# Optimization experiments

Hardware: AMD Instinct MI355X
Metric: run time of the kernel (lower is better)

## Reference

```python
import jax, jax.numpy as jnp
import numpy as np

NUM_CLASSES = 21
TOP_K = 200
CONF_THRESH = 0.01
NMS_THRESH = 0.45
VAR0, VAR1 = 0.1, 0.2
B, P = 64, 8732  # SSD300 VOC prior count


def setup_inputs() -> dict:
    key = jax.random.key(0)
    k1, k2, k3 = jax.random.split(key, 3)
    loc = jax.random.normal(k1, (B, P, 4), dtype=jnp.float32)
    conf = jax.random.normal(k2, (B, P, NUM_CLASSES), dtype=jnp.float32)
    priors = jax.random.uniform(k3, (P, 4), dtype=jnp.float32, minval=0.02, maxval=1.0)
    return {"loc": loc, "conf": conf, "priors": priors}


def _decode(loc, priors):
    # loc, priors: [P, 4] (cx, cy, w, h) offsets -> corner boxes [P, 4]
    cxcy = priors[:, :2] + loc[:, :2] * VAR0 * priors[:, 2:]
    wh = priors[:, 2:] * jnp.exp(loc[:, 2:] * VAR1)
    x1y1 = cxcy - wh * 0.5
    x2y2 = x1y1 + wh
    return jnp.concatenate([x1y1, x2y2], axis=1)


def _iou_matrix(boxes):
    # boxes [K,4] -> pairwise IoU [K,K] with the original +1 pixel convention
    x1, y1, x2, y2 = boxes[:, 0], boxes[:, 1], boxes[:, 2], boxes[:, 3]
    area = (x2 - x1 + 1.0) * (y2 - y1 + 1.0)
    xx1 = jnp.maximum(x1[:, None], x1[None, :])
    yy1 = jnp.maximum(y1[:, None], y1[None, :])
    xx2 = jnp.minimum(x2[:, None], x2[None, :])
    yy2 = jnp.minimum(y2[:, None], y2[None, :])
    w = jnp.maximum(0.0, xx2 - xx1 + 1.0)
    h = jnp.maximum(0.0, yy2 - yy1 + 1.0)
    inter = w * h
    return inter / (area[:, None] + area[None, :] - inter)


def _nms_keep(boxes, valid):
    # boxes [K,4] sorted by descending score; greedy NMS as a fixed-length loop
    K = boxes.shape[0]
    iou = _iou_matrix(boxes)
    later = jnp.arange(K)[None, :] > jnp.arange(K)[:, None]  # strictly lower-priority

    def body(i, suppressed):
        keep_i = valid[i] & ~suppressed[i]
        return suppressed | (keep_i & (iou[i] > NMS_THRESH) & later[i])

    suppressed = jax.lax.fori_loop(0, K, body, jnp.zeros((K,), bool))
    return valid & ~suppressed


def _per_class(scores, decoded):
    # scores [P], decoded [P,4] -> [TOP_K, 7] rows (score, x1, y1, x2, y2, 0, 0)
    valid_p = scores > CONF_THRESH
    s = jnp.where(valid_p, scores, -1.0)
    top_s, idx = jax.lax.top_k(s, TOP_K)
    b = decoded[idx]                      # [K,4]
    valid = top_s > CONF_THRESH
    keep = _nms_keep(b, valid)
    rows = jnp.concatenate([top_s[:, None], b], axis=1)  # [K,5]
    order = jnp.argsort(~keep)            # stable: kept rows compacted to front
    rows = jnp.where(keep[order][:, None], rows[order], 0.0)
    return jnp.pad(rows, ((0, 0), (0, 2)))  # pad to width 7 (original leaves cols 5:7 zero)


def _per_image(loc_i, conf_i, priors):
    decoded = _decode(loc_i, priors)      # [P,4]
    # classes 1..C-1 (skip background class 0)
    cls_scores = conf_i[:, 1:].T          # [C-1, P]
    cls_out = jax.vmap(lambda s: _per_class(s, decoded))(cls_scores)  # [C-1,K,7]
    bg = jnp.zeros((1, TOP_K, 7), dtype=loc_i.dtype)
    return jnp.concatenate([bg, cls_out], axis=0)  # [C,K,7]


def _detect(loc, conf, priors):
    conf_soft = jax.nn.softmax(conf, axis=-1)  # SSD test phase applies softmax
    output = jax.vmap(_per_image, in_axes=(0, 0, None))(loc, conf_soft, priors)  # [B,C,K,7]
    flt = output.reshape(output.shape[0], -1, 7)  # [B, C*K, 7]
    score = flt[:, :, 0]
    idx = jnp.argsort(-score, axis=1)
    rank = jnp.argsort(idx, axis=1)
    mask = rank < TOP_K
    order = jnp.argsort(~mask, axis=1)    # stable: top-K rows, original positional order
    sel = jnp.take_along_axis(flt, order[:, :TOP_K, None], axis=1)  # [B,K,7]
    return sel.reshape(-1, 7)             # [B*K, 7], matching flt[rank < top_k]


def reference(loc, conf, priors):
    return _detect(loc, conf, priors)
```

## Files before the change

kernel.cpp:

```cpp
#include <hip/hip_runtime.h>
#include <stdint.h>

#define NUM_P 8732
#define NUM_B 64
#define NUM_CLS 21
#define TOPK 200
#define NMS_T 0.45f
#define CONF_T 0.01f
#define NL 35
#define NV4 2183
#define NL2 16
#define MAXCAND 4000
#define ORD_SENT 0x407FFFFFu
#define HI_BITS 0x17800u

__device__ __forceinline__ uint32_t ordf(float f) {
    uint32_t u = __float_as_uint(f);
    return (u & 0x80000000u) ? ~u : (u | 0x80000000u);
}
__device__ __forceinline__ float unordf(uint32_t v) {
    uint32_t u = (v & 0x80000000u) ? (v ^ 0x80000000u) : ~v;
    return __uint_as_float(u);
}

__global__ __launch_bounds__(256) void prep_kernel(const float* __restrict__ conf,
                                                   uint32_t* __restrict__ ct,
                                                   uint32_t* __restrict__ candCount) {
    __shared__ float tile[256 * NUM_CLS];
    const int bx = blockIdx.x;
    const int b = blockIdx.y;
    const int tid = threadIdx.x;
    if (bx == 0 && b == 0 && tid < NUM_B) candCount[tid] = 0u;
    const int p0 = bx * 256;
    const int np = min(256, NUM_P - p0);
    const int nf4 = (np * NUM_CLS) / 4;
    const float4* src = reinterpret_cast<const float4*>(conf + ((size_t)b * NUM_P + p0) * NUM_CLS);
    float4* dst = reinterpret_cast<float4*>(tile);
#pragma unroll
    for (int i = 0; i < 6; ++i) {
        int idx = tid + i * 256;
        if (idx < nf4) dst[idx] = src[idx];
    }
    __syncthreads();
    if (tid < np) {
        const int p = p0 + tid;
        const float* row = tile + tid * NUM_CLS;
        float x[NUM_CLS];
#pragma unroll
        for (int c = 0; c < NUM_CLS; ++c) x[c] = row[c];
        float m = x[0];
#pragma unroll
        for (int c = 1; c < NUM_CLS; ++c) m = fmaxf(m, x[c]);
        float e[NUM_CLS];
        float s = 0.0f;
#pragma unroll
        for (int c = 0; c < NUM_CLS; ++c) { e[c] = expf(x[c] - m); s += e[c]; }
#pragma unroll
        for (int c = 1; c < NUM_CLS; ++c) {
            float sc = e[c] / s;
            float sv = (sc > CONF_T) ? sc : -1.0f;
            ct[((size_t)(b * 20 + (c - 1))) * NUM_P + p] = ordf(sv);
        }
    }
}

__global__ __launch_bounds__(256, 4) void select_nms_kernel(const uint32_t* __restrict__ ct,
                                                            const float* __restrict__ loc,
                                                            const float* __restrict__ priors,
                                                            float* __restrict__ selS,
                                                            float* __restrict__ selX1,
                                                            float* __restrict__ selY1,
                                                            float* __restrict__ selX2,
                                                            float* __restrict__ selY2,
                                                            uint64_t* __restrict__ cands,
                                                            uint32_t* __restrict__ candCount) {
    __shared__ uint32_t hist[2048];
    __shared__ uint32_t wtot[4];
    __shared__ uint32_t sh_d, sh_above, sh_bnd, sh_nsent;
    __shared__ uint64_t skey[256];
    __shared__ int scnt;
    __shared__ int sh_run;

    const int blk = blockIdx.x;
    const int b = blk / 20;
    const int c = blk % 20;
    const int tid = threadIdx.x;
    const int lane = tid & 63;
    const int wv = tid >> 6;
    const uint32_t* col = ct + (size_t)blk * NUM_P;
    const uint4* colv = reinterpret_cast<const uint4*>(col);

#pragma unroll
    for (int i = 0; i < 8; ++i) hist[tid + i * 256] = 0;
    skey[tid] = 0;
    if (tid == 0) { scnt = 0; sh_run = 0; }
    __syncthreads();

    uint4 vv[9];
#pragma unroll
    for (int i = 0; i < 9; ++i) {
        int idx = tid + i * 256;
        vv[i] = make_uint4(ORD_SENT, ORD_SENT, ORD_SENT, ORD_SENT);
        if (idx < NV4) vv[i] = colv[idx];
    }
    int nsent = 0;
#pragma unroll
    for (int i = 0; i < 9; ++i) {
        int idx = tid + i * 256;
        if (idx < NV4) {
            uint32_t a0 = vv[i].x, a1 = vv[i].y, a2 = vv[i].z, a3 = vv[i].w;
            if (a0 == ORD_SENT) nsent++; else atomicAdd(&hist[(a0 >> 15) & 2047u], 1u);
            if (a1 == ORD_SENT) nsent++; else atomicAdd(&hist[(a1 >> 15) & 2047u], 1u);
            if (a2 == ORD_SENT) nsent++; else atomicAdd(&hist[(a2 >> 15) & 2047u], 1u);
            if (a3 == ORD_SENT) nsent++; else atomicAdd(&hist[(a3 >> 15) & 2047u], 1u);
        }
    }
    {
        int v = nsent;
#pragma unroll
        for (int off = 32; off; off >>= 1) v += __shfl_down(v, off);
        if (lane == 0) wtot[wv] = (uint32_t)v;
        __syncthreads();
        if (tid == 0) sh_nsent = wtot[0] + wtot[1] + wtot[2] + wtot[3];
        __syncthreads();
    }
    const int nreal = NUM_P - (int)sh_nsent;

    uint32_t emitThr = 0;
    bool ranked = false;
    uint32_t thrEq = 0;
    int needEq = 0;

    if (nreal >= TOPK) {
        {
            const int tbase = tid * 8;
            uint32_t ls = 0;
#pragma unroll
            for (int j = 0; j < 8; ++j) ls += hist[tbase + j];
            uint32_t v = ls;
#pragma unroll
            for (int off = 1; off < 64; off <<= 1) {
                uint32_t o2 = __shfl_down(v, off);
                if (lane + off < 64) v += o2;
            }
            if (lane == 0) wtot[wv] = v;
            __syncthreads();
            uint32_t above_wave = 0;
            for (int w = wv + 1; w < 4; ++w) above_wave += wtot[w];
            uint32_t acc = (v + above_wave) - ls;
            for (int j = 7; j >= 0; --j) {
                uint32_t h = hist[tbase + j];
                if (acc < (uint32_t)TOPK && acc + h >= (uint32_t)TOPK) {
                    sh_d = (uint32_t)(tbase + j);
                    sh_above = acc;
                    sh_bnd = h;
                }
                acc += h;
            }
            __syncthreads();
        }
        uint32_t d1 = sh_d;
        int cert = (int)sh_above;
        int need = TOPK - cert;
        int bnd = (int)sh_bnd;
        const uint32_t lvl1 = HI_BITS | d1;

        if (cert + bnd <= 256) {
            emitThr = lvl1 << 15;
        } else {
            __syncthreads();
#pragma unroll
            for (int i = 0; i < 8; ++i) hist[tid + i * 256] = 0;
            __syncthreads();
#pragma unroll
            for (int i = 0; i < 9; ++i) {
                int idx = tid + i * 256;
                if (idx < NV4) {
                    if ((vv[i].x >> 15) == lvl1) atomicAdd(&hist[(vv[i].x >> 4) & 2047u], 1u);
                    if ((vv[i].y >> 15) == lvl1) atomicAdd(&hist[(vv[i].y >> 4) & 2047u], 1u);
                    if ((vv[i].z >> 15) == lvl1) atomicAdd(&hist[(vv[i].z >> 4) & 2047u], 1u);
                    if ((vv[i].w >> 15) == lvl1) atomicAdd(&hist[(vv[i].w >> 4) & 2047u], 1u);
                }
            }
            __syncthreads();
            {
                const int tbase = tid * 8;
                uint32_t ls = 0;
#pragma unroll
                for (int j = 0; j < 8; ++j) ls += hist[tbase + j];
                uint32_t v = ls;
#pragma unroll
                for (int off = 1; off < 64; off <<= 1) {
                    uint32_t o2 = __shfl_down(v, off);
                    if (lane + off < 64) v += o2;
                }
                if (lane == 0) wtot[wv] = v;
                __syncthreads();
                uint32_t above_wave = 0;
                for (int w = wv + 1; w < 4; ++w) above_wave += wtot[w];
                uint32_t acc = (v + above_wave) - ls;
                for (int j = 7; j >= 0; --j) {
                    uint32_t h = hist[tbase + j];
                    if (acc < (uint32_t)need && acc + h >= (uint32_t)need) {
                        sh_d = (uint32_t)(tbase + j);
                        sh_above = acc;
                        sh_bnd = h;
                    }
                    acc += h;
                }
                __syncthreads();
            }
            uint32_t d2 = sh_d;
            cert += (int)sh_above;
            need -= (int)sh_above;
            bnd = (int)sh_bnd;
            const uint32_t pfx28 = (lvl1 << 11) | d2;

            if (cert + bnd <= 256) {
                emitThr = pfx28 << 4;
            } else {
                __syncthreads();
                if (tid < 16) hist[tid] = 0;
                __syncthreads();
#pragma unroll
                for (int i = 0; i < 9; ++i) {
                    int idx = tid + i * 256;
                    if (idx < NV4) {
                        if ((vv[i].x >> 4) == pfx28) atomicAdd(&hist[vv[i].x & 15u], 1u);
                        if ((vv[i].y >> 4) == pfx28) atomicAdd(&hist[vv[i].y & 15u], 1u);
                        if ((vv[i].z >> 4) == pfx28) atomicAdd(&hist[vv[i].z & 15u], 1u);
                        if ((vv[i].w >> 4) == pfx28) atomicAdd(&hist[vv[i].w & 15u], 1u);
                    }
                }
                __syncthreads();
                if (tid == 0) {
                    uint32_t acc = 0;
                    for (int j = 15; j >= 0; --j) {
                        uint32_t h = hist[j];
                        if (acc < (uint32_t)need && acc + h >= (uint32_t)need) {
                            sh_d = (uint32_t)j; sh_above = acc; sh_bnd = h; break;
                        }
                        acc += h;
                    }
                }
                __syncthreads();
                uint32_t d3 = sh_d;
                cert += (int)sh_above;
                need -= (int)sh_above;
                bnd = (int)sh_bnd;
                const uint32_t pfx32 = (pfx28 << 4) | d3;
                if (cert + bnd <= 256) {
                    emitThr = pfx32;
                } else {
                    ranked = true; thrEq = pfx32; needEq = need;
                }
            }
        }
    } else {
        ranked = true; thrEq = ORD_SENT; needEq = TOPK - nreal;
    }

    if (!ranked) {
#pragma unroll
        for (int i = 0; i < 9; ++i) {
            int idx = tid + i * 256;
            if (idx < NV4) {
                uint32_t aa[4] = {vv[i].x, vv[i].y, vv[i].z, vv[i].w};
#pragma unroll
                for (int j = 0; j < 4; ++j) {
                    uint32_t o = aa[j];
                    if (o >= emitThr) {
                        int s0 = atomicAdd(&scnt, 1);
                        uint32_t p = (uint32_t)(idx * 4 + j);
                        if (s0 < 256)
                            skey[s0] = ((uint64_t)o << 32) | (0xFFFFFFFFu - p);
                    }
                }
            }
        }
        __syncthreads();
    } else {
        for (int i = 0; i < NL; ++i) {
            int p = i * 256 + tid;
            uint32_t o = (p < NUM_P) ? col[p] : 0u;
            if (o > thrEq) {
                int s0 = atomicAdd(&scnt, 1);
                if (s0 < 256)
                    skey[s0] = ((uint64_t)o << 32) | (0xFFFFFFFFu - (uint32_t)p);
            }
            bool tie = (p < NUM_P) && (o == thrEq);
            unsigned long long ball = __ballot(tie);
            if (lane == 0) wtot[wv] = (uint32_t)__popcll(ball);
            __syncthreads();
            int rank = sh_run;
            for (int w = 0; w < wv; ++w) rank += (int)wtot[w];
            rank += __popcll(ball & ((1ull << lane) - 1ull));
            if (tie && rank < needEq) {
                int s0 = atomicAdd(&scnt, 1);
                if (s0 < 256)
                    skey[s0] = ((uint64_t)o << 32) | (0xFFFFFFFFu - (uint32_t)p);
            }
            __syncthreads();
            if (tid == 0) sh_run += (int)(wtot[0] + wtot[1] + wtot[2] + wtot[3]);
            __syncthreads();
        }
    }

    for (int k = 2; k <= 256; k <<= 1) {
        for (int j = k >> 1; j > 0; j >>= 1) {
            int ixj = tid ^ j;
            if (ixj > tid) {
                uint64_t a = skey[tid], bb = skey[ixj];
                bool up = (tid & k) == 0;
                bool sw = up ? (a < bb) : (a > bb);
                if (sw) { skey[tid] = bb; skey[ixj] = a; }
            }
            __syncthreads();
        }
    }

    float* nb = reinterpret_cast<float*>(hist);
    float* dsc = nb;
    float* dx1 = nb + TOPK;
    float* dy1 = nb + 2 * TOPK;
    float* dx2 = nb + 3 * TOPK;
    float* dy2 = nb + 4 * TOPK;
    float* dar = nb + 5 * TOPK;
    if (tid < TOPK) {
        uint64_t k = skey[tid];
        uint32_t p = 0xFFFFFFFFu - (uint32_t)k;
        float msc = unordf((uint32_t)(k >> 32));
        const float4 l4 = reinterpret_cast<const float4*>(loc)[(size_t)b * NUM_P + p];
        const float4 pr = reinterpret_cast<const float4*>(priors)[p];
        float cx = pr.x + (l4.x * 0.1f) * pr.z;
        float cy = pr.y + (l4.y * 0.1f) * pr.w;
        float w  = pr.z * expf(l4.z * 0.2f);
        float h  = pr.w * expf(l4.w * 0.2f);
        float mx1 = cx - w * 0.5f;
        float my1 = cy - h * 0.5f;
        float mx2 = mx1 + w;
        float my2 = my1 + h;
        dsc[tid] = msc; dx1[tid] = mx1; dy1[tid] = my1; dx2[tid] = mx2; dy2[tid] = my2;
        dar[tid] = (mx2 - mx1 + 1.0f) * (my2 - my1 + 1.0f);
    }
    __syncthreads();
    if (wv != 0) return;

    float scs[4], x1s[4], y1s[4], x2s[4], y2s[4], ars[4];
    uint32_t validm = 0, supm = 0;
#pragma unroll
    for (int s = 0; s < 4; ++s) {
        int idx = s * 64 + lane;
        bool v = idx < TOPK;
        scs[s] = v ? dsc[idx] : -1.0f;
        x1s[s] = v ? dx1[idx] : 0.0f;
        y1s[s] = v ? dy1[idx] : 0.0f;
        x2s[s] = v ? dx2[idx] : 0.0f;
        y2s[s] = v ? dy2[idx] : 0.0f;
        ars[s] = v ? dar[idx] : 1.0f;
        if (v && scs[s] > CONF_T) validm |= (1u << s);
    }

#pragma unroll
    for (int slot = 0; slot < 4; ++slot) {
        const int nown = (slot == 3) ? (TOPK - 3 * 64) : 64;
        for (int owner = 0; owner < nown; ++owner) {
            const int i = slot * 64 + owner;
            int myk = (int)((validm >> slot) & 1u) & (int)(((supm >> slot) & 1u) ^ 1u);
            int keep_i = __shfl(myk, owner);
            if (keep_i) {
                float bx1 = __shfl(x1s[slot], owner);
                float by1 = __shfl(y1s[slot], owner);
                float bx2 = __shfl(x2s[slot], owner);
                float by2 = __shfl(y2s[slot], owner);
                float bar_ = __shfl(ars[slot], owner);
#pragma unroll
                for (int s2 = 0; s2 < 4; ++s2) {
                    int idx = s2 * 64 + lane;
                    if (idx > i && idx < TOPK) {
                        float xx1 = fmaxf(bx1, x1s[s2]);
                        float yy1 = fmaxf(by1, y1s[s2]);
                        float xx2 = fminf(bx2, x2s[s2]);
                        float yy2 = fminf(by2, y2s[s2]);
                        float w = fmaxf(0.0f, xx2 - xx1 + 1.0f);
                        float h = fmaxf(0.0f, yy2 - yy1 + 1.0f);
                        float inter = w * h;
                        float iou = inter / (bar_ + ars[s2] - inter);
                        if (iou > NMS_T) supm |= (1u << s2);
                    }
                }
            }
        }
    }

    const size_t base = (size_t)blk * TOPK;
    int off = 0;
    uint64_t wkey[4];
    int wrank[4];
    bool wk[4];
#pragma unroll
    for (int s = 0; s < 4; ++s) {
        int idx = s * 64 + lane;
        bool kept = (idx < TOPK) && ((validm >> s) & 1u) && !((supm >> s) & 1u);
        unsigned long long ball = __ballot(kept);
        int rank = off + __popcll(ball & ((1ull << lane) - 1ull));
        wk[s] = kept;
        wrank[s] = rank;
        wkey[s] = 0;
        if (kept) {
            selS[base + rank] = scs[s];
            selX1[base + rank] = x1s[s];
            selY1[base + rank] = y1s[s];
            selX2[base + rank] = x2s[s];
            selY2[base + rank] = y2s[s];
            uint32_t pos = (uint32_t)(c + 1) * TOPK + (uint32_t)rank;
            wkey[s] = ((uint64_t)ordf(scs[s]) << 32) | (uint32_t)(0xFFFFFFFFu - pos);
        }
        off += __popcll(ball);
    }
    uint32_t bcast = 0;
    if (lane == 0) bcast = atomicAdd(&candCount[b], (uint32_t)off);
    bcast = (uint32_t)__shfl((int)bcast, 0);
#pragma unroll
    for (int s = 0; s < 4; ++s)
        if (wk[s]) cands[(size_t)b * MAXCAND + bcast + wrank[s]] = wkey[s];
}

__global__ __launch_bounds__(256) void final_kernel(const uint64_t* __restrict__ cands,
                                                    const uint32_t* __restrict__ candCount,
                                                    const float* __restrict__ selS,
                                                    const float* __restrict__ selX1,
                                                    const float* __restrict__ selY1,
                                                    const float* __restrict__ selX2,
                                                    const float* __restrict__ selY2,
                                                    float* __restrict__ out) {
    const int b = blockIdx.x;
    const int tid = threadIdx.x;
    const int lane = tid & 63;
    const int wv = tid >> 6;
    const int n = (int)candCount[b];

    uint64_t key[NL2];
#pragma unroll
    for (int i = 0; i < NL2; ++i) {
        int idx = tid + i * 256;
        key[i] = (idx < n) ? cands[(size_t)b * MAXCAND + idx] : 0ull;
    }

    __shared__ int wsum[2][4];
    uint64_t prefix = 0;
    if (n > TOPK) {
        for (int bit = 63; bit >= 0; --bit) {
            uint64_t cand = prefix | (1ull << bit);
            int cnt = 0;
#pragma unroll
            for (int i = 0; i < NL2; ++i) cnt += (key[i] >= cand) ? 1 : 0;
            for (int off = 32; off; off >>= 1) cnt += __shfl_down(cnt, off);
            int bufi = bit & 1;
            if (lane == 0) wsum[bufi][wv] = cnt;
            __syncthreads();
            int tot = wsum[bufi][0] + wsum[bufi][1] + wsum[bufi][2] + wsum[bufi][3];
            if (tot >= TOPK) prefix = cand;
        }
    }

    __shared__ uint32_t selpos[256];
    __shared__ int scnt;
    selpos[tid] = 0xFFFFFFFFu;
    if (tid == 0) scnt = 0;
    __syncthreads();
#pragma unroll
    for (int i = 0; i < NL2; ++i)
        if (key[i] != 0ull && key[i] >= prefix) {
            int s = atomicAdd(&scnt, 1);
            selpos[s] = 0xFFFFFFFFu - (uint32_t)key[i];
        }
    __syncthreads();
    int nsel = scnt;

    for (int k = 2; k <= 256; k <<= 1) {
        for (int j = k >> 1; j > 0; j >>= 1) {
            int ixj = tid ^ j;
            if (ixj > tid) {
                uint32_t a = selpos[tid], bb = selpos[ixj];
                bool up = (tid & k) == 0;
                bool sw = up ? (a > bb) : (a < bb);
                if (sw) { selpos[tid] = bb; selpos[ixj] = a; }
            }
            __syncthreads();
        }
    }

    if (tid < TOPK) {
        int T = TOPK - (nsel < TOPK ? nsel : TOPK);
        float* o = out + ((size_t)b * TOPK + tid) * 7;
        if (tid < T) {
            o[0] = 0.f; o[1] = 0.f; o[2] = 0.f; o[3] = 0.f; o[4] = 0.f; o[5] = 0.f; o[6] = 0.f;
        } else {
            uint32_t pos = selpos[tid - T];
            uint32_t cc = pos / TOPK;
            uint32_t sl = pos % TOPK;
            size_t r = ((size_t)b * 20 + (cc - 1)) * TOPK + sl;
            o[0] = selS[r]; o[1] = selX1[r]; o[2] = selY1[r]; o[3] = selX2[r]; o[4] = selY2[r];
            o[5] = 0.f; o[6] = 0.f;
        }
    }
}

extern "C" void kernel_launch(void* const* d_in, const int* in_sizes, int n_in,
                              void* d_out, int out_size, void* d_ws, size_t ws_size,
                              hipStream_t stream) {
    const float* loc    = (const float*)d_in[0];
    const float* conf   = (const float*)d_in[1];
    const float* priors = (const float*)d_in[2];
    float* out = (float*)d_out;

    const size_t CAND_BYTES = (size_t)NUM_B * MAXCAND * sizeof(uint64_t);
    const size_t SEL_ONE    = (size_t)NUM_B * 20 * TOPK * sizeof(float);
    const size_t CNT_BYTES  = 256;

    char* ws = (char*)d_ws;
    uint64_t* cands     = (uint64_t*)ws;
    float*    selS      = (float*)(ws + CAND_BYTES);
    float*    selX1     = (float*)(ws + CAND_BYTES + SEL_ONE);
    float*    selY1     = (float*)(ws + CAND_BYTES + 2 * SEL_ONE);
    float*    selX2     = (float*)(ws + CAND_BYTES + 3 * SEL_ONE);
    float*    selY2     = (float*)(ws + CAND_BYTES + 4 * SEL_ONE);
    uint32_t* candCount = (uint32_t*)(ws + CAND_BYTES + 5 * SEL_ONE);
    uint32_t* ct        = (uint32_t*)(ws + CAND_BYTES + 5 * SEL_ONE + CNT_BYTES);

    dim3 pgrid((NUM_P + 255) / 256, NUM_B);
    prep_kernel<<<pgrid, 256, 0, stream>>>(conf, ct, candCount);
    select_nms_kernel<<<NUM_B * 20, 256, 0, stream>>>(ct, loc, priors,
                                                      selS, selX1, selY1, selX2, selY2,
                                                      cands, candCount);
    final_kernel<<<NUM_B, 256, 0, stream>>>(cands, candCount,
                                            selS, selX1, selY1, selX2, selY2, out);
}
```

Baseline: 69.99 us.

## Parallelize NMS IoU into bitmask matrix, rank-sort top-K, histogram final select

In the select/NMS kernel, the bitonic sort of candidate keys becomes a rank-by-counting placement. All 256 threads now precompute a 200x200 IoU suppression bitmask in shared memory, so the serial greedy loop in one wave only does bit tests instead of IoU arithmetic. The final kernel swaps the 64-step bitwise radix select for an 11-bit histogram pass, falling back to the old select only when the boundary bucket is large, and swaps the bitonic sort of positions for rank counting. This adds shared memory (colm, extra arrays), which may lower occupancy, and does more total IoU work because the full matrix is computed rather than only rows for kept boxes.

```diff
diff --git a/kernel.cpp b/kernel.cpp
--- a/kernel.cpp
+++ b/kernel.cpp
@@ -75,9 +75,10 @@
                                                             uint64_t* __restrict__ cands,
                                                             uint32_t* __restrict__ candCount) {
     __shared__ uint32_t hist[2048];
+    __shared__ uint64_t skey[256];
+    __shared__ uint64_t colm[TOPK][4];
     __shared__ uint32_t wtot[4];
     __shared__ uint32_t sh_d, sh_above, sh_bnd, sh_nsent;
-    __shared__ uint64_t skey[256];
     __shared__ int scnt;
     __shared__ int sh_run;
 
@@ -306,30 +307,24 @@
         }
     }
 
-    for (int k = 2; k <= 256; k <<= 1) {
-        for (int j = k >> 1; j > 0; j >>= 1) {
-            int ixj = tid ^ j;
-            if (ixj > tid) {
-                uint64_t a = skey[tid], bb = skey[ixj];
-                bool up = (tid & k) == 0;
-                bool sw = up ? (a < bb) : (a > bb);
-                if (sw) { skey[tid] = bb; skey[ixj] = a; }
-            }
-            __syncthreads();
-        }
-    }
-
-    float* nb = reinterpret_cast<float*>(hist);
-    float* dsc = nb;
-    float* dx1 = nb + TOPK;
-    float* dy1 = nb + 2 * TOPK;
-    float* dx2 = nb + 3 * TOPK;
-    float* dy2 = nb + 4 * TOPK;
-    float* dar = nb + 5 * TOPK;
+    uint64_t* skey2 = &colm[0][0];
+    uint64_t myk = skey[tid];
+    skey2[tid] = 0;
+    __syncthreads();
+    int rk = 0;
+#pragma unroll 8
+    for (int j = 0; j < 256; ++j) rk += (skey[j] > myk) ? 1 : 0;
+    if (myk != 0) skey2[rk] = myk;
+    __syncthreads();
+
+    float4* bbox = reinterpret_cast<float4*>(hist);
+    float*  dar  = reinterpret_cast<float*>(hist) + 4 * TOPK;
+    float*  dsc  = reinterpret_cast<float*>(hist) + 5 * TOPK;
+    uint64_t kreg = (tid < TOPK) ? skey2[tid] : 0;
+    __syncthreads();
     if (tid < TOPK) {
-        uint64_t k = skey[tid];
-        uint32_t p = 0xFFFFFFFFu - (uint32_t)k;
-        float msc = unordf((uint32_t)(k >> 32));
+        uint32_t p = 0xFFFFFFFFu - (uint32_t)kreg;
+        float msc = unordf((uint32_t)(kreg >> 32));
         const float4 l4 = reinterpret_cast<const float4*>(loc)[(size_t)b * NUM_P + p];
         const float4 pr = reinterpret_cast<const float4*>(priors)[p];
         float cx = pr.x + (l4.x * 0.1f) * pr.z;
@@ -340,55 +335,65 @@
         float my1 = cy - h * 0.5f;
         float mx2 = mx1 + w;
         float my2 = my1 + h;
-        dsc[tid] = msc; dx1[tid] = mx1; dy1[tid] = my1; dx2[tid] = mx2; dy2[tid] = my2;
+        bbox[tid] = make_float4(mx1, my1, mx2, my2);
         dar[tid] = (mx2 - mx1 + 1.0f) * (my2 - my1 + 1.0f);
+        dsc[tid] = msc;
+    }
+    __syncthreads();
+
+    if (tid < TOPK) {
+        const float4 bj = bbox[tid];
+        const float jar = dar[tid];
+        uint64_t m0 = 0, m1 = 0, m2 = 0, m3 = 0;
+        int i = 0;
+#define IOU_CHUNK(MW, NB)                                                    \
+        for (int b2 = 0; b2 < (NB); ++b2, ++i) {                             \
+            float4 bi = bbox[i];                                             \
+            float xx1 = fmaxf(bi.x, bj.x);                                   \
+            float yy1 = fmaxf(bi.y, bj.y);                                   \
+            float xx2 = fminf(bi.z, bj.z);                                   \
+            float yy2 = fminf(bi.w, bj.w);                                   \
+            float w = fmaxf(0.0f, xx2 - xx1 + 1.0f);                         \
+            float h = fmaxf(0.0f, yy2 - yy1 + 1.0f);                         \
+            float inter = w * h;                                             \
+            float iou = inter / (dar[i] + jar - inter);                      \
+            bool hit = (iou > NMS_T) && (i < tid);                           \
+            MW |= (uint64_t)(hit ? 1u : 0u) << b2;                           \
+        }
+        IOU_CHUNK(m0, 64)
+        IOU_CHUNK(m1, 64)
+        IOU_CHUNK(m2, 64)
+        IOU_CHUNK(m3, 8)
+#undef IOU_CHUNK
+        colm[tid][0] = m0; colm[tid][1] = m1; colm[tid][2] = m2; colm[tid][3] = m3;
     }
     __syncthreads();
     if (wv != 0) return;
 
-    float scs[4], x1s[4], y1s[4], x2s[4], y2s[4], ars[4];
+    uint64_t cm[4][4];
+    float scs[4], x1s[4], y1s[4], x2s[4], y2s[4];
     uint32_t validm = 0, supm = 0;
 #pragma unroll
     for (int s = 0; s < 4; ++s) {
         int idx = s * 64 + lane;
         bool v = idx < TOPK;
+        float4 bx = v ? bbox[idx] : make_float4(0.f, 0.f, 0.f, 0.f);
         scs[s] = v ? dsc[idx] : -1.0f;
-        x1s[s] = v ? dx1[idx] : 0.0f;
-        y1s[s] = v ? dy1[idx] : 0.0f;
-        x2s[s] = v ? dx2[idx] : 0.0f;
-        y2s[s] = v ? dy2[idx] : 0.0f;
-        ars[s] = v ? dar[idx] : 1.0f;
+        x1s[s] = bx.x; y1s[s] = bx.y; x2s[s] = bx.z; y2s[s] = bx.w;
+#pragma unroll
+        for (int w = 0; w < 4; ++w) cm[s][w] = v ? colm[idx][w] : 0;
         if (v && scs[s] > CONF_T) validm |= (1u << s);
     }
-
-#pragma unroll
-    for (int slot = 0; slot < 4; ++slot) {
-        const int nown = (slot == 3) ? (TOPK - 3 * 64) : 64;
-        for (int owner = 0; owner < nown; ++owner) {
-            const int i = slot * 64 + owner;
-            int myk = (int)((validm >> slot) & 1u) & (int)(((supm >> slot) & 1u) ^ 1u);
-            int keep_i = __shfl(myk, owner);
+#pragma unroll
+    for (int w = 0; w < 4; ++w) {
+        const int nb2 = (w == 3) ? (TOPK - 3 * 64) : 64;
+        for (int b2 = 0; b2 < nb2; ++b2) {
+            int myk2 = (int)((validm >> w) & 1u) & (int)(((supm >> w) & 1u) ^ 1u);
+            int keep_i = __shfl(myk2, b2);
             if (keep_i) {
-                float bx1 = __shfl(x1s[slot], owner);
-                float by1 = __shfl(y1s[slot], owner);
-                float bx2 = __shfl(x2s[slot], owner);
-                float by2 = __shfl(y2s[slot], owner);
-                float bar_ = __shfl(ars[slot], owner);
-#pragma unroll
-                for (int s2 = 0; s2 < 4; ++s2) {
-                    int idx = s2 * 64 + lane;
-                    if (idx > i && idx < TOPK) {
-                        float xx1 = fmaxf(bx1, x1s[s2]);
-                        float yy1 = fmaxf(by1, y1s[s2]);
-                        float xx2 = fminf(bx2, x2s[s2]);
-                        float yy2 = fminf(by2, y2s[s2]);
-                        float w = fmaxf(0.0f, xx2 - xx1 + 1.0f);
-                        float h = fmaxf(0.0f, yy2 - yy1 + 1.0f);
-                        float inter = w * h;
-                        float iou = inter / (bar_ + ars[s2] - inter);
-                        if (iou > NMS_T) supm |= (1u << s2);
-                    }
-                }
+#pragma unroll
+                for (int s = 0; s < 4; ++s)
+                    supm |= (uint32_t)((cm[s][w] >> b2) & 1ull) << s;
             }
         }
     }
@@ -434,6 +439,15 @@
                                                     const float* __restrict__ selX2,
                                                     const float* __restrict__ selY2,
                                                     float* __restrict__ out) {
+    __shared__ uint32_t hist[2048];
+    __shared__ uint64_t skey[256];
+    __shared__ uint32_t posArr[TOPK];
+    __shared__ uint32_t sortedPos[TOPK];
+    __shared__ uint32_t wtot[4];
+    __shared__ int wsum[2][4];
+    __shared__ uint32_t sh_d, sh_above, sh_bnd;
+    __shared__ int scnt;
+
     const int b = blockIdx.x;
     const int tid = threadIdx.x;
     const int lane = tid & 63;
@@ -446,58 +460,98 @@
         int idx = tid + i * 256;
         key[i] = (idx < n) ? cands[(size_t)b * MAXCAND + idx] : 0ull;
     }
-
-    __shared__ int wsum[2][4];
-    uint64_t prefix = 0;
+#pragma unroll
+    for (int i = 0; i < 8; ++i) hist[tid + i * 256] = 0;
+    skey[tid] = 0;
+    if (tid == 0) scnt = 0;
+    __syncthreads();
+
+    uint64_t emitThr = 1;
     if (n > TOPK) {
-        for (int bit = 63; bit >= 0; --bit) {
-            uint64_t cand = prefix | (1ull << bit);
-            int cnt = 0;
-#pragma unroll
-            for (int i = 0; i < NL2; ++i) cnt += (key[i] >= cand) ? 1 : 0;
-            for (int off = 32; off; off >>= 1) cnt += __shfl_down(cnt, off);
-            int bufi = bit & 1;
-            if (lane == 0) wsum[bufi][wv] = cnt;
-            __syncthreads();
-            int tot = wsum[bufi][0] + wsum[bufi][1] + wsum[bufi][2] + wsum[bufi][3];
-            if (tot >= TOPK) prefix = cand;
-        }
-    }
-
-    __shared__ uint32_t selpos[256];
-    __shared__ int scnt;
-    selpos[tid] = 0xFFFFFFFFu;
-    if (tid == 0) scnt = 0;
-    __syncthreads();
-#pragma unroll
-    for (int i = 0; i < NL2; ++i)
-        if (key[i] != 0ull && key[i] >= prefix) {
-            int s = atomicAdd(&scnt, 1);
-            selpos[s] = 0xFFFFFFFFu - (uint32_t)key[i];
-        }
-    __syncthreads();
-    int nsel = scnt;
-
-    for (int k = 2; k <= 256; k <<= 1) {
-        for (int j = k >> 1; j > 0; j >>= 1) {
-            int ixj = tid ^ j;
-            if (ixj > tid) {
-                uint32_t a = selpos[tid], bb = selpos[ixj];
-                bool up = (tid & k) == 0;
-                bool sw = up ? (a > bb) : (a < bb);
-                if (sw) { selpos[tid] = bb; selpos[ixj] = a; }
-            }
-            __syncthreads();
-        }
-    }
+#pragma unroll
+        for (int i = 0; i < NL2; ++i)
+            if (key[i] != 0ull) atomicAdd(&hist[(uint32_t)(key[i] >> 47) & 2047u], 1u);
+        __syncthreads();
+        {
+            const int tbase = tid * 8;
+            uint32_t ls = 0;
+#pragma unroll
+            for (int j = 0; j < 8; ++j) ls += hist[tbase + j];
+            uint32_t v = ls;
+#pragma unroll
+            for (int off = 1; off < 64; off <<= 1) {
+                uint32_t o2 = __shfl_down(v, off);
+                if (lane + off < 64) v += o2;
+            }
+            if (lane == 0) wtot[wv] = v;
+            __syncthreads();
+            uint32_t above_wave = 0;
+            for (int w = wv + 1; w < 4; ++w) above_wave += wtot[w];
+            uint32_t acc = (v + above_wave) - ls;
+            for (int j = 7; j >= 0; --j) {
+                uint32_t h = hist[tbase + j];
+                if (acc < (uint32_t)TOPK && acc + h >= (uint32_t)TOPK) {
+                    sh_d = (uint32_t)(tbase + j);
+                    sh_above = acc;
+                    sh_bnd = h;
+                }
+                acc += h;
+            }
+            __syncthreads();
+        }
+        if (sh_above + sh_bnd <= 256u) {
+            emitThr = (uint64_t)(HI_BITS | sh_d) << 47;
+        } else {
+            uint64_t prefix = 0;
+            for (int bit = 63; bit >= 0; --bit) {
+                uint64_t cand = prefix | (1ull << bit);
+                int cnt = 0;
+#pragma unroll
+                for (int i = 0; i < NL2; ++i) cnt += (key[i] >= cand) ? 1 : 0;
+                for (int off = 32; off; off >>= 1) cnt += __shfl_down(cnt, off);
+                int bufi = bit & 1;
+                if (lane == 0) wsum[bufi][wv] = cnt;
+                __syncthreads();
+                int tot = wsum[bufi][0] + wsum[bufi][1] + wsum[bufi][2] + wsum[bufi][3];
+                if (tot >= TOPK) prefix = cand;
+            }
+            emitThr = prefix;
+        }
+    }
+
+#pragma unroll
+    for (int i = 0; i < NL2; ++i) {
+        if (key[i] != 0ull && key[i] >= emitThr) {
+            int s0 = atomicAdd(&scnt, 1);
+            if (s0 < 256) skey[s0] = key[i];
+        }
+    }
+    __syncthreads();
+    const int nsel = min(scnt, TOPK);
+
+    uint64_t myk = skey[tid];
+    __syncthreads();
+    int rk = 0;
+#pragma unroll 8
+    for (int j = 0; j < 256; ++j) rk += (skey[j] > myk) ? 1 : 0;
+    if (myk != 0 && rk < TOPK) posArr[rk] = 0xFFFFFFFFu - (uint32_t)myk;
+    __syncthreads();
+
+    if (tid < nsel) {
+        uint32_t mypos = posArr[tid];
+        int pr = 0;
+        for (int j = 0; j < nsel; ++j) pr += (posArr[j] < mypos) ? 1 : 0;
+        sortedPos[pr] = mypos;
+    }
+    __syncthreads();
 
     if (tid < TOPK) {
-        int T = TOPK - (nsel < TOPK ? nsel : TOPK);
+        int T = TOPK - nsel;
         float* o = out + ((size_t)b * TOPK + tid) * 7;
         if (tid < T) {
             o[0] = 0.f; o[1] = 0.f; o[2] = 0.f; o[3] = 0.f; o[4] = 0.f; o[5] = 0.f; o[6] = 0.f;
         } else {
-            uint32_t pos = selpos[tid - T];
+            uint32_t pos = sortedPos[tid - T];
             uint32_t cc = pos / TOPK;
             uint32_t sl = pos % TOPK;
             size_t r = ((size_t)b * 20 + (cc - 1)) * TOPK + sl;
```

Result: slower. 112.1 us (+60.1%).
